# Kernel tuning notes

Hardware: AMD Instinct MI355X
Metric: run time of the kernel (lower is better)

Reference implementation:

```python
import math
import jax, jax.numpy as jnp
import numpy as np

B, C, H, W = 8, 512, 32, 32
N_HEADS = 8
N_GROUPS = 32  # GroupNorm(32) as in guided-diffusion normalization()
EPS = 1e-5


def setup_inputs() -> dict:
    key = jax.random.key(0)
    k0, k1, k2, k3, k4 = jax.random.split(key, 5)
    x = jax.random.normal(k0, (B, C, H, W), dtype=jnp.float32)
    gn_scale = jnp.ones((C,), dtype=jnp.float32)
    gn_bias = jnp.zeros((C,), dtype=jnp.float32)
    # 1x1 conv weights stored as (out, in); proj_out is zero-initialized in the
    # original but we use small random weights so the op is non-trivial.
    qkv_w = jax.random.normal(k1, (3 * C, C), dtype=jnp.float32) * 0.02
    qkv_b = jax.random.normal(k2, (3 * C,), dtype=jnp.float32) * 0.02
    proj_w = jax.random.normal(k3, (C, C), dtype=jnp.float32) * 0.02
    proj_b = jax.random.normal(k4, (C,), dtype=jnp.float32) * 0.02
    return {"x": x, "gn_scale": gn_scale, "gn_bias": gn_bias,
            "qkv_w": qkv_w, "qkv_b": qkv_b, "proj_w": proj_w, "proj_b": proj_b}


def reference(x, gn_scale, gn_bias, qkv_w, qkv_b, proj_w, proj_b):
    b, c, h, w = x.shape
    L = h * w
    xf = x.reshape(b, c, L)

    # GroupNorm(32): normalize over (channels-in-group, length)
    xg = xf.reshape(b, N_GROUPS, c // N_GROUPS, L)
    mu = jnp.mean(xg, axis=(2, 3), keepdims=True)
    var = jnp.var(xg, axis=(2, 3), keepdims=True)
    xn = ((xg - mu) * jax.lax.rsqrt(var + EPS)).reshape(b, c, L)
    xn = xn * gn_scale[None, :, None] + gn_bias[None, :, None]

    # 1x1 conv -> qkv (b, 3c, L)
    qkv = jnp.einsum('oc,bcl->bol', qkv_w, xn) + qkv_b[None, :, None]

    ch = c // N_HEADS  # head dim (width//(3*n_heads) of qkv)
    q, k, v = jnp.split(qkv, 3, axis=1)
    q = q.reshape(b * N_HEADS, ch, L)
    k = k.reshape(b * N_HEADS, ch, L)
    v = v.reshape(b * N_HEADS, ch, L)

    scale = 1.0 / math.sqrt(math.sqrt(ch))
    # scores: (b*heads, L, L) materialized, as in the original
    wts = jnp.einsum('bct,bcs->bts', q * scale, k * scale)
    wts = jax.nn.softmax(wts.astype(jnp.float32), axis=-1).astype(q.dtype)
    a = jnp.einsum('bts,bcs->bct', wts, v).reshape(b, c, L)

    # zero-initialized 1x1 proj in original; random weights here
    hout = jnp.einsum('oc,bcl->bol', proj_w, a) + proj_b[None, :, None]
    return (xf + hout).reshape(b, c, h, w)
```

## Files before the change

### kernel.cpp

```cpp
#include <hip/hip_runtime.h>
#include <math.h>

#define BATCH   8
#define CCH     512
#define LL      1024
#define NHEADS  8
#define CHD     64
#define EPSV    1e-5f
#define QSCALE  0.1803368801111204f

typedef __bf16 bf16_t;
typedef bf16_t bf16x8 __attribute__((ext_vector_type(8)));
typedef bf16_t bf16x4 __attribute__((ext_vector_type(4)));
typedef float  f32x4  __attribute__((ext_vector_type(4)));

__device__ __forceinline__ bf16_t f2b(float f) {
  unsigned u = __float_as_uint(f);
  u += 0x7fff + ((u >> 16) & 1);
  return __builtin_bit_cast(bf16_t, (unsigned short)(u >> 16));
}

__device__ __forceinline__ unsigned pack2(float lo, float hi) {
  unsigned a = (unsigned)__builtin_bit_cast(unsigned short, f2b(lo));
  unsigned b = (unsigned)__builtin_bit_cast(unsigned short, f2b(hi));
  return (b << 16) | a;
}

__device__ __forceinline__ void gload_lds16(const void* g, void* l) {
  __builtin_amdgcn_global_load_lds(
      (const __attribute__((address_space(1))) void*)g,
      (__attribute__((address_space(3))) void*)l, 16, 0, 0);
}

__global__ __launch_bounds__(256) void gn_stats(const float* __restrict__ x,
                                                float* __restrict__ stats) {
  int bg = blockIdx.x;
  const float4* x4 = (const float4*)(x + (size_t)bg * 16 * LL);
  int tid = threadIdx.x;
  float s = 0.f, ss = 0.f;
#pragma unroll
  for (int it = 0; it < 16; ++it) {
    float4 f = x4[it * 256 + tid];
    s += f.x + f.y + f.z + f.w;
    ss += f.x * f.x + f.y * f.y + f.z * f.z + f.w * f.w;
  }
#pragma unroll
  for (int m = 1; m < 64; m <<= 1) { s += __shfl_xor(s, m); ss += __shfl_xor(ss, m); }
  __shared__ float rs_[4], rss[4];
  int wv = tid >> 6, ln = tid & 63;
  if (ln == 0) { rs_[wv] = s; rss[wv] = ss; }
  __syncthreads();
  if (tid == 0) {
    float S = rs_[0] + rs_[1] + rs_[2] + rs_[3];
    float SS = rss[0] + rss[1] + rss[2] + rss[3];
    float mean = S * (1.f / 16384.f);
    float var = SS * (1.f / 16384.f) - mean * mean;
    stats[bg * 2] = mean;
    stats[bg * 2 + 1] = rsqrtf(var + EPSV);
  }
}

__global__ __launch_bounds__(256) void norm_t(const float* __restrict__ x,
                                              const float* __restrict__ stats,
                                              const float* __restrict__ gsc,
                                              const float* __restrict__ gbi,
                                              bf16_t* __restrict__ xnT) {
  __shared__ bf16_t T[64 * 40];
  int b = blockIdx.z, c0 = blockIdx.y * 32, l0 = blockIdx.x * 64;
  int tid = threadIdx.x;
#pragma unroll
  for (int p = 0; p < 2; ++p) {
    int idx = p * 256 + tid;
    int c = idx >> 4, l4 = idx & 15;
    int cg = c0 + c;
    float4 v = *(const float4*)(x + ((size_t)(b * CCH + cg)) * LL + l0 + l4 * 4);
    int g = cg >> 4;
    float mean = stats[(b * 32 + g) * 2];
    float rstd = stats[(b * 32 + g) * 2 + 1];
    float sc = gsc[cg] * rstd;
    float bi = gbi[cg] - mean * sc;
    T[(l4 * 4 + 0) * 40 + c] = f2b(v.x * sc + bi);
    T[(l4 * 4 + 1) * 40 + c] = f2b(v.y * sc + bi);
    T[(l4 * 4 + 2) * 40 + c] = f2b(v.z * sc + bi);
    T[(l4 * 4 + 3) * 40 + c] = f2b(v.w * sc + bi);
  }
  __syncthreads();
  int l = tid >> 2, seg = tid & 3;
  bf16x8 val = *(const bf16x8*)&T[l * 40 + seg * 8];
  *(bf16x8*)(xnT + ((size_t)b * LL + l0 + l) * CCH + c0 + seg * 8) = val;
}

__global__ __launch_bounds__(256) void cvt_bf16(const float* __restrict__ src,
                                                bf16_t* __restrict__ dst, int n) {
  int i = (blockIdx.x * 256 + threadIdx.x) * 4;
  if (i < n) {
    float4 v = *(const float4*)(src + i);
    bf16x4 o = {f2b(v.x), f2b(v.y), f2b(v.z), f2b(v.w)};
    *(bf16x4*)(dst + i) = o;
  }
}

__global__ __launch_bounds__(256) void qkv_mfma(const bf16_t* __restrict__ wq,
                                                const bf16_t* __restrict__ xnT,
                                                const float* __restrict__ qkvb,
                                                bf16_t* __restrict__ qt,
                                                bf16_t* __restrict__ kt,
                                                bf16_t* __restrict__ vt) {
  __shared__ bf16_t As[128 * 64];
  __shared__ bf16_t Bs[128 * 64];
  int tid = threadIdx.x;
  int wave = tid >> 6, lane = tid & 63;
  int lrow = lane & 15, quad = lane >> 4;
  int wm = wave >> 1, wn = wave & 1;
  int b = blockIdx.x;
  int oBase = blockIdx.y * 128, lBase = blockIdx.z * 128;
  int srow = lane >> 3;
  int sgOff = (((lane & 7) ^ srow) << 4);

  f32x4 acc[4][4] = {};
  for (int ktile = 0; ktile < 8; ++ktile) {
    int kB = ktile * 64;
    __syncthreads();
#pragma unroll
    for (int j = 0; j < 4; ++j) {
      int ci = wave * 4 + j;
      int R = ci * 8 + srow;
      gload_lds16((const char*)(wq + (size_t)(oBase + R) * CCH + kB) + sgOff,
                  (char*)As + ci * 1024);
      gload_lds16((const char*)(xnT + ((size_t)b * LL + lBase + R) * CCH + kB) + sgOff,
                  (char*)Bs + ci * 1024);
    }
    __syncthreads();
#pragma unroll
    for (int kk = 0; kk < 2; ++kk) {
      bf16x8 af[4], bfr[4];
#pragma unroll
      for (int m = 0; m < 4; ++m) {
        int r = wm * 64 + m * 16 + lrow;
        int g = (kk * 4 + quad) ^ (lrow & 7);
        af[m] = *(const bf16x8*)(As + r * 64 + g * 8);
      }
#pragma unroll
      for (int n = 0; n < 4; ++n) {
        int r = wn * 64 + n * 16 + lrow;
        int g = (kk * 4 + quad) ^ (lrow & 7);
        bfr[n] = *(const bf16x8*)(Bs + r * 64 + g * 8);
      }
#pragma unroll
      for (int m = 0; m < 4; ++m)
#pragma unroll
        for (int n = 0; n < 4; ++n)
          acc[m][n] = __builtin_amdgcn_mfma_f32_16x16x32_bf16(af[m], bfr[n], acc[m][n], 0, 0, 0);
    }
  }

  int oW = oBase + wm * 64;
  int lW = lBase + wn * 64;
  int sec = oW >> 9;
#pragma unroll
  for (int m = 0; m < 4; ++m) {
    int o4 = oW + m * 16 + quad * 4;
    float4 bb4 = *(const float4*)&qkvb[o4];
    int cc = o4 & 511;
    int head = cc >> 6, ch = cc & 63;
    int bh = b * NHEADS + head;
    if (sec == 0) {
#pragma unroll
      for (int n = 0; n < 4; ++n) {
        int l = lW + n * 16 + lrow;
        unsigned d0 = pack2((acc[m][n][0] + bb4.x) * QSCALE,
                            (acc[m][n][1] + bb4.y) * QSCALE);
        unsigned d1 = pack2((acc[m][n][2] + bb4.z) * QSCALE,
                            (acc[m][n][3] + bb4.w) * QSCALE);
        *(uint2*)(qt + ((size_t)bh * LL + l) * CHD + ch) = make_uint2(d0, d1);
      }
    } else if (sec == 1) {
#pragma unroll
      for (int n = 0; n < 4; ++n) {
        int l = lW + n * 16 + lrow;
        unsigned d0 = pack2(acc[m][n][0] + bb4.x, acc[m][n][1] + bb4.y);
        unsigned d1 = pack2(acc[m][n][2] + bb4.z, acc[m][n][3] + bb4.w);
        *(uint2*)(kt + ((size_t)bh * LL + l) * CHD + ch) = make_uint2(d0, d1);
      }
    } else {
      float bb[4] = {bb4.x, bb4.y, bb4.z, bb4.w};
#pragma unroll
      for (int i = 0; i < 4; ++i) {
        unsigned d0 = pack2(acc[m][0][i] + bb[i], acc[m][1][i] + bb[i]);
        unsigned d1 = pack2(acc[m][2][i] + bb[i], acc[m][3][i] + bb[i]);
        *(uint2*)(vt + ((size_t)bh * CHD + ch + i) * LL + lW + lrow * 4) =
            make_uint2(d0, d1);
      }
    }
  }
}

__global__ __launch_bounds__(256) void attn_mfma(const bf16_t* __restrict__ qt,
                                                 const bf16_t* __restrict__ kt,
                                                 const bf16_t* __restrict__ vt,
                                                 bf16_t* __restrict__ at) {
  __shared__ bf16_t kbuf[2][64 * 64];
  __shared__ bf16_t vbuf[2][64 * 64];
  __shared__ bf16_t pb[4 * 16 * 72];
  int tid = threadIdx.x, wave = tid >> 6, lane = tid & 63;
  int lrow = lane & 15, quad = lane >> 4;
  int bh = blockIdx.x;
  int tW = blockIdx.y * 64 + wave * 16;
  const bf16_t* qb = qt + (size_t)bh * LL * CHD;
  const bf16_t* kb = kt + (size_t)bh * LL * CHD;
  const bf16_t* vb = vt + (size_t)bh * CHD * LL;
  bf16_t* pw = pb + wave * 16 * 72;

  int srow = lane >> 3;
  int sgb = (((lane & 7) ^ srow) << 4);

  bf16x8 qf0 = *(const bf16x8*)(qb + (size_t)(tW + lrow) * CHD + quad * 8);
  bf16x8 qf1 = *(const bf16x8*)(qb + (size_t)(tW + lrow) * CHD + 32 + quad * 8);

  bf16x8 ones;
#pragma unroll
  for (int j = 0; j < 8; ++j) ones[j] = (bf16_t)1.0f;

  f32x4 Oa[4] = {};
  f32x4 Os = {};

#pragma unroll
  for (int j = 0; j < 2; ++j) {
    int c = wave * 2 + j;
    int R = c * 8 + srow;
    gload_lds16((const char*)(kb + (size_t)R * CHD) + sgb, (char*)&kbuf[0][0] + c * 1024);
    gload_lds16((const char*)(vb + (size_t)R * LL) + sgb, (char*)&vbuf[0][0] + c * 1024);
  }
  __syncthreads();

  int swz0 = (quad ^ (lrow & 7)) * 8;
  int swz1 = ((quad + 4) ^ (lrow & 7)) * 8;

  for (int st = 0; st < 16; ++st) {
    int cur = st & 1;
    if (st < 15) {
      int sBn = (st + 1) * 64;
#pragma unroll
      for (int j = 0; j < 2; ++j) {
        int c = wave * 2 + j;
        int R = c * 8 + srow;
        gload_lds16((const char*)(kb + (size_t)(sBn + R) * CHD) + sgb,
                    (char*)&kbuf[cur ^ 1][0] + c * 1024);
        gload_lds16((const char*)(vb + (size_t)R * LL + sBn) + sgb,
                    (char*)&vbuf[cur ^ 1][0] + c * 1024);
      }
    }
    const bf16_t* kbase = &kbuf[cur][0];
    const bf16_t* vbase = &vbuf[cur][0];

    f32x4 S[4];
#pragma unroll
    for (int ss = 0; ss < 4; ++ss) {
      int s = ss * 16 + lrow;
      bf16x8 k0 = *(const bf16x8*)(kbase + s * 64 + swz0);
      bf16x8 k1 = *(const bf16x8*)(kbase + s * 64 + swz1);
      f32x4 z = {0.f, 0.f, 0.f, 0.f};
      z = __builtin_amdgcn_mfma_f32_16x16x32_bf16(qf0, k0, z, 0, 0, 0);
      S[ss] = __builtin_amdgcn_mfma_f32_16x16x32_bf16(qf1, k1, z, 0, 0, 0);
    }

    float p[4][4];
#pragma unroll
    for (int ss = 0; ss < 4; ++ss)
#pragma unroll
      for (int i = 0; i < 4; ++i)
        p[ss][i] = __builtin_amdgcn_exp2f(S[ss][i]);
#pragma unroll
    for (int i = 0; i < 4; ++i) {
      unsigned d0 = __builtin_amdgcn_perm(__float_as_uint(p[1][i]),
                                          __float_as_uint(p[0][i]), 0x07060302u);
      unsigned d1 = __builtin_amdgcn_perm(__float_as_uint(p[3][i]),
                                          __float_as_uint(p[2][i]), 0x07060302u);
      uint2* dst = (uint2*)(pw + (quad * 4 + i) * 72 + lrow * 4);
      *dst = make_uint2(d0, d1);
    }
    asm volatile("s_waitcnt lgkmcnt(0)" ::: "memory");

    bf16x8 pf0 = *(const bf16x8*)(pw + lrow * 72 + quad * 8);
    bf16x8 pf1 = *(const bf16x8*)(pw + lrow * 72 + 32 + quad * 8);

#pragma unroll
    for (int n = 0; n < 4; ++n) {
      int r = (n * 16 + lrow) * 64;
      bf16x8 v0 = *(const bf16x8*)(vbase + r + swz0);
      bf16x8 v1 = *(const bf16x8*)(vbase + r + swz1);
      Oa[n] = __builtin_amdgcn_mfma_f32_16x16x32_bf16(pf0, v0, Oa[n], 0, 0, 0);
      Oa[n] = __builtin_amdgcn_mfma_f32_16x16x32_bf16(pf1, v1, Oa[n], 0, 0, 0);
    }
    Os = __builtin_amdgcn_mfma_f32_16x16x32_bf16(pf0, ones, Os, 0, 0, 0);
    Os = __builtin_amdgcn_mfma_f32_16x16x32_bf16(pf1, ones, Os, 0, 0, 0);

    __syncthreads();
  }

  float inv[4];
#pragma unroll
  for (int i = 0; i < 4; ++i) inv[i] = 1.f / Os[i];
  bf16_t* ab = at + (size_t)bh * LL * CHD;
#pragma unroll
  for (int n = 0; n < 4; ++n)
#pragma unroll
    for (int i = 0; i < 4; ++i)
      ab[(size_t)(tW + quad * 4 + i) * CHD + n * 16 + lrow] = f2b(Oa[n][i] * inv[i]);
}

__global__ __launch_bounds__(256) void proj_mfma(const bf16_t* __restrict__ wp,
                                                 const bf16_t* __restrict__ at,
                                                 const float* __restrict__ projb,
                                                 const float* __restrict__ x,
                                                 float* __restrict__ out) {
  __shared__ bf16_t As[128 * 64];
  __shared__ bf16_t Bs[128 * 64];
  int tid = threadIdx.x;
  int wave = tid >> 6, lane = tid & 63;
  int lrow = lane & 15, quad = lane >> 4;
  int wm = wave >> 1, wn = wave & 1;
  int b = blockIdx.x;
  int oBase = blockIdx.y * 128, lBase = blockIdx.z * 128;
  int srow = lane >> 3;
  int sgOff = (((lane & 7) ^ srow) << 4);

  f32x4 acc[4][4] = {};
  for (int ktile = 0; ktile < 8; ++ktile) {
    int kB = ktile * 64;
    __syncthreads();
#pragma unroll
    for (int j = 0; j < 4; ++j) {
      int ci = wave * 4 + j;
      int R = ci * 8 + srow;
      gload_lds16((const char*)(wp + (size_t)(oBase + R) * CCH + kB) + sgOff,
                  (char*)As + ci * 1024);
      gload_lds16((const char*)(at + ((size_t)(b * NHEADS + ktile) * LL + lBase + R) * CHD) + sgOff,
                  (char*)Bs + ci * 1024);
    }
    __syncthreads();
#pragma unroll
    for (int kk = 0; kk < 2; ++kk) {
      bf16x8 af[4], bfr[4];
#pragma unroll
      for (int m = 0; m < 4; ++m) {
        int r = wm * 64 + m * 16 + lrow;
        int g = (kk * 4 + quad) ^ (lrow & 7);
        af[m] = *(const bf16x8*)(As + r * 64 + g * 8);
      }
#pragma unroll
      for (int n = 0; n < 4; ++n) {
        int r = wn * 64 + n * 16 + lrow;
        int g = (kk * 4 + quad) ^ (lrow & 7);
        bfr[n] = *(const bf16x8*)(Bs + r * 64 + g * 8);
      }
#pragma unroll
      for (int m = 0; m < 4; ++m)
#pragma unroll
        for (int n = 0; n < 4; ++n)
          acc[m][n] = __builtin_amdgcn_mfma_f32_16x16x32_bf16(af[m], bfr[n], acc[m][n], 0, 0, 0);
    }
  }

  int oW = oBase + wm * 64;
  int lW = lBase + wn * 64;
#pragma unroll
  for (int m = 0; m < 4; ++m) {
#pragma unroll
    for (int i = 0; i < 4; ++i) {
      int o = oW + m * 16 + quad * 4 + i;
      float bb = projb[o];
#pragma unroll
      for (int n = 0; n < 4; ++n) {
        int l = lW + n * 16 + lrow;
        size_t off = ((size_t)(b * CCH + o)) * LL + l;
        out[off] = acc[m][n][i] + bb + x[off];
      }
    }
  }
}

extern "C" void kernel_launch(void* const* d_in, const int* in_sizes, int n_in,
                              void* d_out, int out_size, void* d_ws, size_t ws_size,
                              hipStream_t stream) {
  const float* x     = (const float*)d_in[0];
  const float* gsc   = (const float*)d_in[1];
  const float* gbi   = (const float*)d_in[2];
  const float* qkvw  = (const float*)d_in[3];
  const float* qkvb  = (const float*)d_in[4];
  const float* projw = (const float*)d_in[5];
  const float* projb = (const float*)d_in[6];
  float* out = (float*)d_out;

  char* ws = (char*)d_ws;
  float*  stats = (float*)ws;
  bf16_t* wqb   = (bf16_t*)(ws + 4096);
  bf16_t* wpb   = (bf16_t*)(ws + 4096 + 1572864);
  bf16_t* xnT   = (bf16_t*)(ws + 2101248);
  bf16_t* qt    = (bf16_t*)(ws + 2101248 + 8388608);
  bf16_t* kt    = (bf16_t*)(ws + 2101248 + 2 * 8388608);
  bf16_t* vt    = (bf16_t*)(ws + 2101248 + 3 * 8388608);
  bf16_t* at    = (bf16_t*)(ws + 2101248 + 4 * 8388608);

  hipLaunchKernelGGL(cvt_bf16, dim3(768), dim3(256), 0, stream, qkvw, wqb, 1536 * 512);
  hipLaunchKernelGGL(cvt_bf16, dim3(256), dim3(256), 0, stream, projw, wpb, 512 * 512);
  hipLaunchKernelGGL(gn_stats, dim3(256), dim3(256), 0, stream, x, stats);
  hipLaunchKernelGGL(norm_t, dim3(16, 16, BATCH), dim3(256), 0, stream,
                     x, stats, gsc, gbi, xnT);
  hipLaunchKernelGGL(qkv_mfma, dim3(BATCH, 12, 8), dim3(256), 0, stream,
                     wqb, xnT, qkvb, qt, kt, vt);
  hipLaunchKernelGGL(attn_mfma, dim3(64, 16), dim3(256), 0, stream, qt, kt, vt, at);
  hipLaunchKernelGGL(proj_mfma, dim3(BATCH, 4, 8), dim3(256), 0, stream,
                     wpb, at, projb, x, out);
}
```

Baseline: 172.1 us.

## Fuse GroupNorm stats and normalize-transpose; double query rows per attention wave

Merges the GroupNorm statistics kernel and the normalize/transpose kernel into one kernel that keeps each group's 16 channels in registers, computes mean/rstd, and writes the transposed bf16 rows directly. This removes one launch and a second read of x, with block indexing remapped across XCDs. The attention kernel now has each wave handle 32 query rows instead of 16, so each K/V tile loaded into LDS is reused twice as much. The cost is half as many attention blocks (512) and higher register pressure from the doubled accumulators.

Measured after the change: 162.3 us. 5.7% less time.

```diff
diff --git a/kernel.cpp b/kernel.cpp
--- a/kernel.cpp
+++ b/kernel.cpp
@@ -32,15 +32,23 @@
       (__attribute__((address_space(3))) void*)l, 16, 0, 0);
 }
 
-__global__ __launch_bounds__(256) void gn_stats(const float* __restrict__ x,
-                                                float* __restrict__ stats) {
-  int bg = blockIdx.x;
-  const float4* x4 = (const float4*)(x + (size_t)bg * 16 * LL);
+__global__ __launch_bounds__(256) void gn_norm(const float* __restrict__ x,
+                                               const float* __restrict__ gsc,
+                                               const float* __restrict__ gbi,
+                                               bf16_t* __restrict__ xnT) {
+  int lin = blockIdx.x;
+  int xcd = lin & 7, slot = lin >> 3;
+  int b = slot & 7, jj = slot >> 3;
+  int g = xcd * 4 + jj;
+  const float4* x4 = (const float4*)(x + ((size_t)(b * 32 + g)) * 16 * LL);
   int tid = threadIdx.x;
+
   float s = 0.f, ss = 0.f;
+  float4 v[16];
 #pragma unroll
   for (int it = 0; it < 16; ++it) {
     float4 f = x4[it * 256 + tid];
+    v[it] = f;
     s += f.x + f.y + f.z + f.w;
     ss += f.x * f.x + f.y * f.y + f.z * f.z + f.w * f.w;
   }
@@ -50,44 +58,33 @@
   int wv = tid >> 6, ln = tid & 63;
   if (ln == 0) { rs_[wv] = s; rss[wv] = ss; }
   __syncthreads();
-  if (tid == 0) {
-    float S = rs_[0] + rs_[1] + rs_[2] + rs_[3];
-    float SS = rss[0] + rss[1] + rss[2] + rss[3];
-    float mean = S * (1.f / 16384.f);
-    float var = SS * (1.f / 16384.f) - mean * mean;
-    stats[bg * 2] = mean;
-    stats[bg * 2 + 1] = rsqrtf(var + EPSV);
-  }
-}
-
-__global__ __launch_bounds__(256) void norm_t(const float* __restrict__ x,
-                                              const float* __restrict__ stats,
-                                              const float* __restrict__ gsc,
-                                              const float* __restrict__ gbi,
-                                              bf16_t* __restrict__ xnT) {
-  __shared__ bf16_t T[64 * 40];
-  int b = blockIdx.z, c0 = blockIdx.y * 32, l0 = blockIdx.x * 64;
-  int tid = threadIdx.x;
-#pragma unroll
-  for (int p = 0; p < 2; ++p) {
-    int idx = p * 256 + tid;
-    int c = idx >> 4, l4 = idx & 15;
-    int cg = c0 + c;
-    float4 v = *(const float4*)(x + ((size_t)(b * CCH + cg)) * LL + l0 + l4 * 4);
-    int g = cg >> 4;
-    float mean = stats[(b * 32 + g) * 2];
-    float rstd = stats[(b * 32 + g) * 2 + 1];
-    float sc = gsc[cg] * rstd;
-    float bi = gbi[cg] - mean * sc;
-    T[(l4 * 4 + 0) * 40 + c] = f2b(v.x * sc + bi);
-    T[(l4 * 4 + 1) * 40 + c] = f2b(v.y * sc + bi);
-    T[(l4 * 4 + 2) * 40 + c] = f2b(v.z * sc + bi);
-    T[(l4 * 4 + 3) * 40 + c] = f2b(v.w * sc + bi);
-  }
-  __syncthreads();
-  int l = tid >> 2, seg = tid & 3;
-  bf16x8 val = *(const bf16x8*)&T[l * 40 + seg * 8];
-  *(bf16x8*)(xnT + ((size_t)b * LL + l0 + l) * CCH + c0 + seg * 8) = val;
+  s  = rs_[0] + rs_[1] + rs_[2] + rs_[3];
+  ss = rss[0] + rss[1] + rss[2] + rss[3];
+  float mean = s * (1.f / 16384.f);
+  float var  = ss * (1.f / 16384.f) - mean * mean;
+  float rstd = rsqrtf(var + EPSV);
+
+  float sc[16], bi[16];
+#pragma unroll
+  for (int it = 0; it < 16; ++it) {
+    sc[it] = gsc[g * 16 + it] * rstd;
+    bi[it] = gbi[g * 16 + it] - mean * sc[it];
+  }
+
+#pragma unroll
+  for (int j = 0; j < 4; ++j) {
+    unsigned w[8];
+#pragma unroll
+    for (int k = 0; k < 8; ++k) {
+      float a0 = (j == 0 ? v[2 * k].x : j == 1 ? v[2 * k].y : j == 2 ? v[2 * k].z : v[2 * k].w);
+      float a1 = (j == 0 ? v[2 * k + 1].x : j == 1 ? v[2 * k + 1].y : j == 2 ? v[2 * k + 1].z : v[2 * k + 1].w);
+      w[k] = pack2(a0 * sc[2 * k] + bi[2 * k], a1 * sc[2 * k + 1] + bi[2 * k + 1]);
+    }
+    int l = tid * 4 + j;
+    bf16_t* dst = xnT + ((size_t)b * LL + l) * CCH + g * 16;
+    *(uint4*)dst = make_uint4(w[0], w[1], w[2], w[3]);
+    *(uint4*)(dst + 8) = make_uint4(w[4], w[5], w[6], w[7]);
+  }
 }
 
 __global__ __launch_bounds__(256) void cvt_bf16(const float* __restrict__ src,
@@ -201,28 +198,32 @@
                                                  bf16_t* __restrict__ at) {
   __shared__ bf16_t kbuf[2][64 * 64];
   __shared__ bf16_t vbuf[2][64 * 64];
-  __shared__ bf16_t pb[4 * 16 * 72];
+  __shared__ bf16_t pb[8 * 16 * 72];
   int tid = threadIdx.x, wave = tid >> 6, lane = tid & 63;
   int lrow = lane & 15, quad = lane >> 4;
   int bh = blockIdx.x;
-  int tW = blockIdx.y * 64 + wave * 16;
+  int tW = blockIdx.y * 128 + wave * 32;
   const bf16_t* qb = qt + (size_t)bh * LL * CHD;
   const bf16_t* kb = kt + (size_t)bh * LL * CHD;
   const bf16_t* vb = vt + (size_t)bh * CHD * LL;
-  bf16_t* pw = pb + wave * 16 * 72;
 
   int srow = lane >> 3;
   int sgb = (((lane & 7) ^ srow) << 4);
 
-  bf16x8 qf0 = *(const bf16x8*)(qb + (size_t)(tW + lrow) * CHD + quad * 8);
-  bf16x8 qf1 = *(const bf16x8*)(qb + (size_t)(tW + lrow) * CHD + 32 + quad * 8);
+  bf16x8 qf[2][2];
+#pragma unroll
+  for (int h = 0; h < 2; ++h) {
+    const bf16_t* qp = qb + (size_t)(tW + h * 16 + lrow) * CHD + quad * 8;
+    qf[h][0] = *(const bf16x8*)qp;
+    qf[h][1] = *(const bf16x8*)(qp + 32);
+  }
 
   bf16x8 ones;
 #pragma unroll
   for (int j = 0; j < 8; ++j) ones[j] = (bf16_t)1.0f;
 
-  f32x4 Oa[4] = {};
-  f32x4 Os = {};
+  f32x4 Oa[2][4] = {};
+  f32x4 Os[2] = {};
 
 #pragma unroll
   for (int j = 0; j < 2; ++j) {
@@ -253,60 +254,82 @@
     const bf16_t* kbase = &kbuf[cur][0];
     const bf16_t* vbase = &vbuf[cur][0];
 
-    f32x4 S[4];
+    f32x4 S[2][4];
 #pragma unroll
     for (int ss = 0; ss < 4; ++ss) {
       int s = ss * 16 + lrow;
       bf16x8 k0 = *(const bf16x8*)(kbase + s * 64 + swz0);
       bf16x8 k1 = *(const bf16x8*)(kbase + s * 64 + swz1);
-      f32x4 z = {0.f, 0.f, 0.f, 0.f};
-      z = __builtin_amdgcn_mfma_f32_16x16x32_bf16(qf0, k0, z, 0, 0, 0);
-      S[ss] = __builtin_amdgcn_mfma_f32_16x16x32_bf16(qf1, k1, z, 0, 0, 0);
-    }
-
-    float p[4][4];
-#pragma unroll
-    for (int ss = 0; ss < 4; ++ss)
-#pragma unroll
-      for (int i = 0; i < 4; ++i)
-        p[ss][i] = __builtin_amdgcn_exp2f(S[ss][i]);
-#pragma unroll
-    for (int i = 0; i < 4; ++i) {
-      unsigned d0 = __builtin_amdgcn_perm(__float_as_uint(p[1][i]),
-                                          __float_as_uint(p[0][i]), 0x07060302u);
-      unsigned d1 = __builtin_amdgcn_perm(__float_as_uint(p[3][i]),
-                                          __float_as_uint(p[2][i]), 0x07060302u);
-      uint2* dst = (uint2*)(pw + (quad * 4 + i) * 72 + lrow * 4);
-      *dst = make_uint2(d0, d1);
+#pragma unroll
+      for (int h = 0; h < 2; ++h) {
+        f32x4 z = {0.f, 0.f, 0.f, 0.f};
+        z = __builtin_amdgcn_mfma_f32_16x16x32_bf16(qf[h][0], k0, z, 0, 0, 0);
+        S[h][ss] = __builtin_amdgcn_mfma_f32_16x16x32_bf16(qf[h][1], k1, z, 0, 0, 0);
+      }
+    }
+
+#pragma unroll
+    for (int h = 0; h < 2; ++h) {
+      bf16_t* pw = pb + (wave * 2 + h) * (16 * 72);
+      float p[4][4];
+#pragma unroll
+      for (int ss = 0; ss < 4; ++ss)
+#pragma unroll
+        for (int i = 0; i < 4; ++i)
+          p[ss][i] = __builtin_amdgcn_exp2f(S[h][ss][i]);
+#pragma unroll
+      for (int i = 0; i < 4; ++i) {
+        unsigned d0 = __builtin_amdgcn_perm(__float_as_uint(p[1][i]),
+                                            __float_as_uint(p[0][i]), 0x07060302u);
+        unsigned d1 = __builtin_amdgcn_perm(__float_as_uint(p[3][i]),
+                                            __float_as_uint(p[2][i]), 0x07060302u);
+        uint2* dst = (uint2*)(pw + (quad * 4 + i) * 72 + lrow * 4);
+        *dst = make_uint2(d0, d1);
+      }
     }
     asm volatile("s_waitcnt lgkmcnt(0)" ::: "memory");
 
-    bf16x8 pf0 = *(const bf16x8*)(pw + lrow * 72 + quad * 8);
-    bf16x8 pf1 = *(const bf16x8*)(pw + lrow * 72 + 32 + quad * 8);
+    bf16x8 pf[2][2];
+#pragma unroll
+    for (int h = 0; h < 2; ++h) {
+      const bf16_t* pw = pb + (wave * 2 + h) * (16 * 72);
+      pf[h][0] = *(const bf16x8*)(pw + lrow * 72 + quad * 8);
+      pf[h][1] = *(const bf16x8*)(pw + lrow * 72 + 32 + quad * 8);
+    }
 
 #pragma unroll
     for (int n = 0; n < 4; ++n) {
       int r = (n * 16 + lrow) * 64;
       bf16x8 v0 = *(const bf16x8*)(vbase + r + swz0);
       bf16x8 v1 = *(const bf16x8*)(vbase + r + swz1);
-      Oa[n] = __builtin_amdgcn_mfma_f32_16x16x32_bf16(pf0, v0, Oa[n], 0, 0, 0);
-      Oa[n] = __builtin_amdgcn_mfma_f32_16x16x32_bf16(pf1, v1, Oa[n], 0, 0, 0);
-    }
-    Os = __builtin_amdgcn_mfma_f32_16x16x32_bf16(pf0, ones, Os, 0, 0, 0);
-    Os = __builtin_amdgcn_mfma_f32_16x16x32_bf16(pf1, ones, Os, 0, 0, 0);
+#pragma unroll
+      for (int h = 0; h < 2; ++h) {
+        Oa[h][n] = __builtin_amdgcn_mfma_f32_16x16x32_bf16(pf[h][0], v0, Oa[h][n], 0, 0, 0);
+        Oa[h][n] = __builtin_amdgcn_mfma_f32_16x16x32_bf16(pf[h][1], v1, Oa[h][n], 0, 0, 0);
+      }
+    }
+#pragma unroll
+    for (int h = 0; h < 2; ++h) {
+      Os[h] = __builtin_amdgcn_mfma_f32_16x16x32_bf16(pf[h][0], ones, Os[h], 0, 0, 0);
+      Os[h] = __builtin_amdgcn_mfma_f32_16x16x32_bf16(pf[h][1], ones, Os[h], 0, 0, 0);
+    }
 
     __syncthreads();
   }
 
-  float inv[4];
-#pragma unroll
-  for (int i = 0; i < 4; ++i) inv[i] = 1.f / Os[i];
   bf16_t* ab = at + (size_t)bh * LL * CHD;
 #pragma unroll
-  for (int n = 0; n < 4; ++n)
-#pragma unroll
-    for (int i = 0; i < 4; ++i)
-      ab[(size_t)(tW + quad * 4 + i) * CHD + n * 16 + lrow] = f2b(Oa[n][i] * inv[i]);
+  for (int h = 0; h < 2; ++h) {
+    float inv[4];
+#pragma unroll
+    for (int i = 0; i < 4; ++i) inv[i] = 1.f / Os[h][i];
+#pragma unroll
+    for (int n = 0; n < 4; ++n)
+#pragma unroll
+      for (int i = 0; i < 4; ++i)
+        ab[(size_t)(tW + h * 16 + quad * 4 + i) * CHD + n * 16 + lrow] =
+            f2b(Oa[h][n][i] * inv[i]);
+  }
 }
 
 __global__ __launch_bounds__(256) void proj_mfma(const bf16_t* __restrict__ wp,
@@ -393,7 +416,6 @@
   float* out = (float*)d_out;
 
   char* ws = (char*)d_ws;
-  float*  stats = (float*)ws;
   bf16_t* wqb   = (bf16_t*)(ws + 4096);
   bf16_t* wpb   = (bf16_t*)(ws + 4096 + 1572864);
   bf16_t* xnT   = (bf16_t*)(ws + 2101248);
@@ -404,12 +426,10 @@
 
   hipLaunchKernelGGL(cvt_bf16, dim3(768), dim3(256), 0, stream, qkvw, wqb, 1536 * 512);
   hipLaunchKernelGGL(cvt_bf16, dim3(256), dim3(256), 0, stream, projw, wpb, 512 * 512);
-  hipLaunchKernelGGL(gn_stats, dim3(256), dim3(256), 0, stream, x, stats);
-  hipLaunchKernelGGL(norm_t, dim3(16, 16, BATCH), dim3(256), 0, stream,
-                     x, stats, gsc, gbi, xnT);
+  hipLaunchKernelGGL(gn_norm, dim3(256), dim3(256), 0, stream, x, gsc, gbi, xnT);
   hipLaunchKernelGGL(qkv_mfma, dim3(BATCH, 12, 8), dim3(256), 0, stream,
                      wqb, xnT, qkvb, qt, kt, vt);
-  hipLaunchKernelGGL(attn_mfma, dim3(64, 16), dim3(256), 0, stream, qt, kt, vt, at);
+  hipLaunchKernelGGL(attn_mfma, dim3(64, 8), dim3(256), 0, stream, qt, kt, vt, at);
   hipLaunchKernelGGL(proj_mfma, dim3(BATCH, 4, 8), dim3(256), 0, stream,
                      wpb, at, projb, x, out);
 }
```
